# Kernel optimization log

Measured on AMD Instinct MI355X. Metric: run time of the kernel, lower is better.

## Reference

```python
import jax, jax.numpy as jnp
import numpy as np

LAMBDA = 10.0
BETA = 10.0
W = 5  # window size per axis (5,5,5); padding=2 hardcoded in original
DN = ('NCDHW', 'OIDHW', 'NCDHW')


def box_mean(x):
    """Uniform 5x5x5 box-filter mean with zero padding=2, via separable 1D convs."""
    specs = [((1, 1, W, 1, 1), [(2, 2), (0, 0), (0, 0)]),
             ((1, 1, 1, W, 1), [(0, 0), (2, 2), (0, 0)]),
             ((1, 1, 1, 1, W), [(0, 0), (0, 0), (2, 2)])]
    for kshape, pads in specs:
        k = jnp.full(kshape, 1.0 / W, dtype=x.dtype)
        x = jax.lax.conv_general_dilated(x, k, (1, 1, 1), pads, dimension_numbers=DN)
    return x


def lcc_loss(gt, pred):
    omega = gt.size
    d_gt = gt - box_mean(gt)
    d_pred = pred - box_mean(pred)
    num = jnp.square(jnp.sum(d_gt * d_pred))
    den = jnp.sum(jnp.square(d_gt)) * jnp.sum(jnp.square(d_pred))
    den = jnp.maximum(den, 1e-5)
    return -(1.0 / omega) * (num / den)


def reg_field_loss(reg_gt, reg_pred):
    omega = reg_gt.size
    return jnp.sqrt(jnp.sum(jnp.square(reg_pred - reg_gt))) / omega


def tversky_loss2(seg_gt, seg_pred):
    den = jnp.maximum(jnp.sum(seg_gt + seg_pred), 1e-5)
    return -0.5 * jnp.sum(2.0 * seg_gt * seg_pred) / den


def setup_inputs() -> dict:
    key = jax.random.key(0)
    ks = jax.random.split(key, 10)
    shp_f = (2, 3, 128, 128, 128)
    shp_i = (2, 1, 128, 128, 128)
    return {
        'F_0': jax.random.normal(ks[0], shp_f, jnp.float32),
        'F_0g': jax.random.normal(ks[1], shp_f, jnp.float32),
        'I_0': jax.random.uniform(ks[2], shp_i, jnp.float32),
        'I_0R': jax.random.uniform(ks[3], shp_i, jnp.float32),
        'I_1': jax.random.uniform(ks[4], shp_i, jnp.float32),
        'I_1R': jax.random.uniform(ks[5], shp_i, jnp.float32),
        'S_0': jax.random.uniform(ks[6], shp_i, jnp.float32),
        'S_0g': jax.random.uniform(ks[7], shp_i, jnp.float32),
        'S_1': jax.random.uniform(ks[8], shp_i, jnp.float32),
        'S_1g': jax.random.uniform(ks[9], shp_i, jnp.float32),
    }


def reference(F_0, F_0g, I_0, I_0R, I_1, I_1R, S_0, S_0g, S_1, S_1g):
    return (reg_field_loss(F_0, F_0g)
            + LAMBDA * (lcc_loss(I_0, I_0R) + lcc_loss(I_1, I_1R))
            + BETA * (tversky_loss2(S_0, S_0g) + tversky_loss2(S_1, S_1g)))
```

## Files before the change

kernel.cpp:

```cpp
#include <hip/hip_runtime.h>
#include <math.h>

#define VOL   (128*128*128)
#define PLANE (128*128)

#define LCC_BLOCKS   1024
#define SQ_BLOCKS    1024
#define TV_BLOCKS    256
#define TOTAL_BLOCKS (LCC_BLOCKS + SQ_BLOCKS + 2 * TV_BLOCKS)

__device__ __forceinline__ void bar_lds_only() {
    asm volatile("s_waitcnt lgkmcnt(0)");
    __builtin_amdgcn_s_barrier();
}


__device__ __forceinline__ double wave_reduce_d(double v) {
    #pragma unroll
    for (int off = 32; off > 0; off >>= 1)
        v += __shfl_down(v, off, 64);
    return v;
}

__device__ __forceinline__ void block_reduce1_atomic(double a, double* dst) {
    __shared__ double s1[4];
    int lane = threadIdx.x & 63;
    int wave = threadIdx.x >> 6;
    a = wave_reduce_d(a);
    if (lane == 0) s1[wave] = a;
    __syncthreads();
    if (threadIdx.x == 0) {
        double A = s1[0] + s1[1] + s1[2] + s1[3];
        atomicAdd(&dst[0], A);
    }
}

__device__ __forceinline__ void block_reduce2_atomic(double a, double b, double* dst) {
    __shared__ double s2[2][4];
    int lane = threadIdx.x & 63;
    int wave = threadIdx.x >> 6;
    a = wave_reduce_d(a);
    b = wave_reduce_d(b);
    if (lane == 0) { s2[0][wave] = a; s2[1][wave] = b; }
    __syncthreads();
    if (threadIdx.x == 0) {
        atomicAdd(&dst[0], s2[0][0] + s2[0][1] + s2[0][2] + s2[0][3]);
        atomicAdd(&dst[1], s2[1][0] + s2[1][1] + s2[1][2] + s2[1][3]);
    }
}

__device__ __forceinline__ void block_reduce3_atomic(double a, double b, double c, double* dst) {
    __shared__ double s3[3][4];
    int lane = threadIdx.x & 63;
    int wave = threadIdx.x >> 6;
    a = wave_reduce_d(a);
    b = wave_reduce_d(b);
    c = wave_reduce_d(c);
    if (lane == 0) { s3[0][wave] = a; s3[1][wave] = b; s3[2][wave] = c; }
    __syncthreads();
    if (threadIdx.x == 0) {
        atomicAdd(&dst[0], s3[0][0] + s3[0][1] + s3[0][2] + s3[0][3]);
        atomicAdd(&dst[1], s3[1][0] + s3[1][1] + s3[1][2] + s3[1][3]);
        atomicAdd(&dst[2], s3[2][0] + s3[2][1] + s3[2][2] + s3[2][3]);
    }
}


__global__ void zero_ws_kernel(double* ws) {
    if (threadIdx.x < 16) ws[threadIdx.x] = 0.0;
}


__global__ __launch_bounds__(256) void mega_kernel(
    const float* __restrict__ F0,  const float* __restrict__ F0g,
    const float* __restrict__ I0,  const float* __restrict__ I0R,
    const float* __restrict__ I1,  const float* __restrict__ I1R,
    const float* __restrict__ S0,  const float* __restrict__ S0g,
    const float* __restrict__ S1,  const float* __restrict__ S1g,
    double* __restrict__ ws)
{
    int b = blockIdx.x;
    int tid = threadIdx.x;

    if (b < LCC_BLOCKS) {
        __shared__ float ybuf[2 * 8 * 128];
        __shared__ float dbuf[8 * 128];

        int pair = b >> 9;
        int r  = b & 511;
        int y0 = (r & 15) << 3;
        int z0 = ((r >> 4) & 15) << 3;
        int n  = r >> 8;

        const float* gt = pair ? I1  : I0;
        const float* pr = pair ? I1R : I0R;
        double* dst = ws + (pair ? 4 : 1);

        int x = tid & 127;
        int g = tid >> 7;
        const float* V = (g ? pr : gt) + (size_t)n * VOL;

        float a1 = 0.f, a2 = 0.f, a3 = 0.f;
        float ps[5][8];
        float cent1[8], cent2[8];
        float v[12];

        float* yb = ybuf + g * 1024;

        {
            int zp = z0 - 2;
            bool zin = (zp >= 0);
            #pragma unroll
            for (int j = 0; j < 12; ++j) {
                int gy = y0 - 2 + j;
                v[j] = (zin && gy >= 0 && gy < 128)
                         ? V[(size_t)zp * PLANE + (size_t)gy * 128 + x] : 0.0f;
            }
        }

        #pragma unroll
        for (int it = 0; it < 12; ++it) {
            int zp = z0 - 2 + it;

            float vn[12];
            if (it < 11) {
                int zq = zp + 1;
                bool zok = (zq >= 0) && (zq < 128);
                #pragma unroll
                for (int j = 0; j < 12; ++j) {
                    int gy = y0 - 2 + j;
                    vn[j] = (zok && gy >= 0 && gy < 128)
                              ? V[(size_t)zq * PLANE + (size_t)gy * 128 + x] : 0.0f;
                }
            }

            #pragma unroll
            for (int k = 0; k < 8; ++k)
                yb[k * 128 + x] = v[k] + v[k+1] + v[k+2] + v[k+3] + v[k+4];

            bar_lds_only();

            #pragma unroll
            for (int k = 0; k < 8; ++k) {
                float s = yb[k * 128 + x];
                if (x >= 2)   s += yb[k * 128 + x - 2];
                if (x >= 1)   s += yb[k * 128 + x - 1];
                if (x <= 126) s += yb[k * 128 + x + 1];
                if (x <= 125) s += yb[k * 128 + x + 2];
                ps[it % 5][k] = s;
            }

            float d[8];
            if (it >= 4) {
                #pragma unroll
                for (int k = 0; k < 8; ++k) {
                    float m = (ps[0][k] + ps[1][k] + ps[2][k] + ps[3][k] + ps[4][k])
                              * (1.0f / 125.0f);
                    d[k] = cent2[k] - m;
                }
                if (g) {
                    #pragma unroll
                    for (int k = 0; k < 8; ++k) {
                        dbuf[k * 128 + x] = d[k];
                        a3 += d[k] * d[k];
                    }
                }
            }

            bar_lds_only();

            if (it >= 4 && g == 0) {
                #pragma unroll
                for (int k = 0; k < 8; ++k) {
                    float dp = dbuf[k * 128 + x];
                    a1 += d[k] * dp;
                    a2 += d[k] * d[k];
                }
            }

            #pragma unroll
            for (int k = 0; k < 8; ++k) { cent2[k] = cent1[k]; cent1[k] = v[k + 2]; }
            if (it < 11) {
                #pragma unroll
                for (int j = 0; j < 12; ++j) v[j] = vn[j];
            }
        }
        block_reduce3_atomic((double)a1, (double)a2, (double)a3, dst);

    } else if (b < LCC_BLOCKS + SQ_BLOCKS) {
        int bid = b - LCC_BLOCKS;
        const float4* A = (const float4*)F0;
        const float4* B = (const float4*)F0g;
        int n4 = 12582912 / 4;
        int idx = bid * 256 + tid;
        int stride = SQ_BLOCKS * 256;
        float acc = 0.f;
        #pragma unroll 4
        for (int i = idx; i < n4; i += stride) {
            float4 xx = A[i], yy = B[i];
            float d0 = yy.x - xx.x, d1 = yy.y - xx.y;
            float d2 = yy.z - xx.z, d3 = yy.w - xx.w;
            acc += (d0 * d0 + d1 * d1) + (d2 * d2 + d3 * d3);
        }
        block_reduce1_atomic((double)acc, &ws[0]);

    } else {
        int bid = b - (LCC_BLOCKS + SQ_BLOCKS);
        int pair = bid >= TV_BLOCKS;
        bid -= pair ? TV_BLOCKS : 0;
        const float4* Gp = (const float4*)(pair ? S1 : S0);
        const float4* Pp = (const float4*)(pair ? S1g : S0g);
        double* dst = ws + (pair ? 9 : 7);
        int n4 = 4194304 / 4;
        int idx = bid * 256 + tid;
        int stride = TV_BLOCKS * 256;
        float asum = 0.f, aprod = 0.f;
        #pragma unroll 4
        for (int i = idx; i < n4; i += stride) {
            float4 xx = Gp[i], yy = Pp[i];
            asum  += (xx.x + yy.x) + (xx.y + yy.y) + (xx.z + yy.z) + (xx.w + yy.w);
            aprod += (xx.x * yy.x + xx.y * yy.y) + (xx.z * yy.z + xx.w * yy.w);
        }
        block_reduce2_atomic((double)asum, (double)aprod, dst);
    }
}

__global__ void finalize_kernel(const double* __restrict__ ws, float* out) {
    if (threadIdx.x == 0 && blockIdx.x == 0) {
        double reg = sqrt(ws[0]) / 12582912.0;

        double num0 = ws[1] * ws[1];
        double den0 = ws[2] * ws[3];
        if (den0 < 1e-5) den0 = 1e-5;
        double l0 = -(1.0 / 4194304.0) * (num0 / den0);

        double num1 = ws[4] * ws[4];
        double den1 = ws[5] * ws[6];
        if (den1 < 1e-5) den1 = 1e-5;
        double l1 = -(1.0 / 4194304.0) * (num1 / den1);

        double td0 = ws[7]; if (td0 < 1e-5) td0 = 1e-5;
        double t0 = -ws[8] / td0;
        double td1 = ws[9]; if (td1 < 1e-5) td1 = 1e-5;
        double t1 = -ws[10] / td1;

        out[0] = (float)(reg + 10.0 * (l0 + l1) + 10.0 * (t0 + t1));
    }
}


extern "C" void kernel_launch(void* const* d_in, const int* in_sizes, int n_in,
                              void* d_out, int out_size, void* d_ws, size_t ws_size,
                              hipStream_t stream) {
    double* ws = (double*)d_ws;
    float* out = (float*)d_out;

    const float* F0  = (const float*)d_in[0];
    const float* F0g = (const float*)d_in[1];
    const float* I0  = (const float*)d_in[2];
    const float* I0R = (const float*)d_in[3];
    const float* I1  = (const float*)d_in[4];
    const float* I1R = (const float*)d_in[5];
    const float* S0  = (const float*)d_in[6];
    const float* S0g = (const float*)d_in[7];
    const float* S1  = (const float*)d_in[8];
    const float* S1g = (const float*)d_in[9];

    zero_ws_kernel<<<1, 64, 0, stream>>>(ws);
    mega_kernel<<<TOTAL_BLOCKS, 256, 0, stream>>>(F0, F0g, I0, I0R, I1, I1R,
                                                  S0, S0g, S1, S1g, ws);
    finalize_kernel<<<1, 64, 0, stream>>>(ws, out);
}
```

Before: 270.7 us.

## Interleave gt/pred lanes and use shuffles instead of LDS exchange barrier

Gt and pred threads for the same x column are now interleaved as adjacent lanes, so the product of deviations is exchanged with a lane shuffle instead of an LDS buffer and a second barrier per z step. The y-sum buffer is double-buffered across iterations so a single barrier per step suffices, and each thread keeps its own center y-sum in registers to save one LDS read. The global loads now have pairs of lanes reading the same address, which halves effective coalescing width. Accumulation uses mask multiplies to avoid divergence.

```diff
diff --git a/kernel.cpp b/kernel.cpp
--- a/kernel.cpp
+++ b/kernel.cpp
@@ -10,7 +10,7 @@
 #define TOTAL_BLOCKS (LCC_BLOCKS + SQ_BLOCKS + 2 * TV_BLOCKS)
 
 __device__ __forceinline__ void bar_lds_only() {
-    asm volatile("s_waitcnt lgkmcnt(0)");
+    asm volatile("s_waitcnt lgkmcnt(0)" ::: "memory");
     __builtin_amdgcn_s_barrier();
 }
 
@@ -83,8 +83,7 @@
     int tid = threadIdx.x;
 
     if (b < LCC_BLOCKS) {
-        __shared__ float ybuf[2 * 8 * 128];
-        __shared__ float dbuf[8 * 128];
+        __shared__ float ybuf[2][2][8][128];
 
         int pair = b >> 9;
         int r  = b & 511;
@@ -96,16 +95,16 @@
         const float* pr = pair ? I1R : I0R;
         double* dst = ws + (pair ? 4 : 1);
 
-        int x = tid & 127;
-        int g = tid >> 7;
+        int g  = tid & 1;
+        int xp = tid >> 1;
         const float* V = (g ? pr : gt) + (size_t)n * VOL;
+        const float gm  = g ? 0.0f : 1.0f;
+        const float gmi = g ? 1.0f : 0.0f;
 
         float a1 = 0.f, a2 = 0.f, a3 = 0.f;
         float ps[5][8];
         float cent1[8], cent2[8];
-        float v[12];
-
-        float* yb = ybuf + g * 1024;
+        float v[12], ybk[8];
 
         {
             int zp = z0 - 2;
@@ -114,7 +113,7 @@
             for (int j = 0; j < 12; ++j) {
                 int gy = y0 - 2 + j;
                 v[j] = (zin && gy >= 0 && gy < 128)
-                         ? V[(size_t)zp * PLANE + (size_t)gy * 128 + x] : 0.0f;
+                         ? V[(size_t)zp * PLANE + (size_t)gy * 128 + xp] : 0.0f;
             }
         }
 
@@ -130,51 +129,42 @@
                 for (int j = 0; j < 12; ++j) {
                     int gy = y0 - 2 + j;
                     vn[j] = (zok && gy >= 0 && gy < 128)
-                              ? V[(size_t)zq * PLANE + (size_t)gy * 128 + x] : 0.0f;
+                              ? V[(size_t)zq * PLANE + (size_t)gy * 128 + xp] : 0.0f;
                 }
             }
 
-            #pragma unroll
-            for (int k = 0; k < 8; ++k)
-                yb[k * 128 + x] = v[k] + v[k+1] + v[k+2] + v[k+3] + v[k+4];
+            float* yb = &ybuf[it & 1][g][0][0];
+            #pragma unroll
+            for (int k = 0; k < 8; ++k) {
+                float s = v[k] + v[k+1] + v[k+2] + v[k+3] + v[k+4];
+                ybk[k] = s;
+                yb[k * 128 + xp] = s;
+            }
 
             bar_lds_only();
 
             #pragma unroll
             for (int k = 0; k < 8; ++k) {
-                float s = yb[k * 128 + x];
-                if (x >= 2)   s += yb[k * 128 + x - 2];
-                if (x >= 1)   s += yb[k * 128 + x - 1];
-                if (x <= 126) s += yb[k * 128 + x + 1];
-                if (x <= 125) s += yb[k * 128 + x + 2];
+                float s = ybk[k];
+                if (xp >= 2)   s += yb[k * 128 + xp - 2];
+                if (xp >= 1)   s += yb[k * 128 + xp - 1];
+                if (xp <= 126) s += yb[k * 128 + xp + 1];
+                if (xp <= 125) s += yb[k * 128 + xp + 2];
                 ps[it % 5][k] = s;
             }
 
-            float d[8];
             if (it >= 4) {
                 #pragma unroll
                 for (int k = 0; k < 8; ++k) {
                     float m = (ps[0][k] + ps[1][k] + ps[2][k] + ps[3][k] + ps[4][k])
                               * (1.0f / 125.0f);
-                    d[k] = cent2[k] - m;
-                }
-                if (g) {
-                    #pragma unroll
-                    for (int k = 0; k < 8; ++k) {
-                        dbuf[k * 128 + x] = d[k];
-                        a3 += d[k] * d[k];
-                    }
-                }
-            }
-
-            bar_lds_only();
-
-            if (it >= 4 && g == 0) {
-                #pragma unroll
-                for (int k = 0; k < 8; ++k) {
-                    float dp = dbuf[k * 128 + x];
-                    a1 += d[k] * dp;
-                    a2 += d[k] * d[k];
+                    float d  = cent2[k] - m;
+                    float dp = __shfl_xor(d, 1, 64);
+                    float prod = d * dp;
+                    float sq   = d * d;
+                    a1 += prod * gm;
+                    a2 += sq   * gm;
+                    a3 += sq   * gmi;
                 }
             }
 
```

Result: slower. 282.7 us (+4.4%).

## Deepen z-plane prefetch to two planes and remap LCC block order

Applied to the files above, without the earlier changes.

The LCC stencil loop now keeps a three-slot register ring of z-planes and prefetches two planes ahead instead of one, so global loads have more iterations to land before use. It also keeps the center y-sum in registers instead of re-reading it from LDS, adds a memory clobber to the LDS barrier asm, and permutes the block index so consecutive blocks cover different tiles. The deeper prefetch raises register pressure and may lower occupancy, and the block permutation changes the cache and XCD locality pattern.

```diff
diff --git a/kernel.cpp b/kernel.cpp
--- a/kernel.cpp
+++ b/kernel.cpp
@@ -10,7 +10,7 @@
 #define TOTAL_BLOCKS (LCC_BLOCKS + SQ_BLOCKS + 2 * TV_BLOCKS)
 
 __device__ __forceinline__ void bar_lds_only() {
-    asm volatile("s_waitcnt lgkmcnt(0)");
+    asm volatile("s_waitcnt lgkmcnt(0)" ::: "memory");
     __builtin_amdgcn_s_barrier();
 }
 
@@ -86,8 +86,10 @@
         __shared__ float ybuf[2 * 8 * 128];
         __shared__ float dbuf[8 * 128];
 
-        int pair = b >> 9;
-        int r  = b & 511;
+        int L = (b & 7) * 128 + (b >> 3);
+
+        int pair = L >> 9;
+        int r  = L & 511;
         int y0 = (r & 15) << 3;
         int z0 = ((r >> 4) & 15) << 3;
         int n  = r >> 8;
@@ -103,46 +105,52 @@
         float a1 = 0.f, a2 = 0.f, a3 = 0.f;
         float ps[5][8];
         float cent1[8], cent2[8];
-        float v[12];
+        float vp[3][12];
+        float ybk[8];
 
         float* yb = ybuf + g * 1024;
 
-        {
-            int zp = z0 - 2;
+        #pragma unroll
+        for (int s = 0; s < 2; ++s) {
+            int zp = z0 - 2 + s;
             bool zin = (zp >= 0);
             #pragma unroll
             for (int j = 0; j < 12; ++j) {
                 int gy = y0 - 2 + j;
-                v[j] = (zin && gy >= 0 && gy < 128)
-                         ? V[(size_t)zp * PLANE + (size_t)gy * 128 + x] : 0.0f;
+                vp[s][j] = (zin && gy >= 0 && gy < 128)
+                             ? V[(size_t)zp * PLANE + (size_t)gy * 128 + x] : 0.0f;
             }
         }
 
         #pragma unroll
         for (int it = 0; it < 12; ++it) {
-            int zp = z0 - 2 + it;
-
-            float vn[12];
-            if (it < 11) {
-                int zq = zp + 1;
-                bool zok = (zq >= 0) && (zq < 128);
+            const int cur = it % 3;
+            const int nxt = (it + 2) % 3;
+
+            if (it < 10) {
+                int zq = z0 + it;
+                bool zok = (zq < 128);
                 #pragma unroll
                 for (int j = 0; j < 12; ++j) {
                     int gy = y0 - 2 + j;
-                    vn[j] = (zok && gy >= 0 && gy < 128)
-                              ? V[(size_t)zq * PLANE + (size_t)gy * 128 + x] : 0.0f;
-                }
-            }
-
-            #pragma unroll
-            for (int k = 0; k < 8; ++k)
-                yb[k * 128 + x] = v[k] + v[k+1] + v[k+2] + v[k+3] + v[k+4];
+                    vp[nxt][j] = (zok && gy >= 0 && gy < 128)
+                                   ? V[(size_t)zq * PLANE + (size_t)gy * 128 + x] : 0.0f;
+                }
+            }
+
+            #pragma unroll
+            for (int k = 0; k < 8; ++k) {
+                float s = vp[cur][k] + vp[cur][k+1] + vp[cur][k+2]
+                        + vp[cur][k+3] + vp[cur][k+4];
+                ybk[k] = s;
+                yb[k * 128 + x] = s;
+            }
 
             bar_lds_only();
 
             #pragma unroll
             for (int k = 0; k < 8; ++k) {
-                float s = yb[k * 128 + x];
+                float s = ybk[k];
                 if (x >= 2)   s += yb[k * 128 + x - 2];
                 if (x >= 1)   s += yb[k * 128 + x - 1];
                 if (x <= 126) s += yb[k * 128 + x + 1];
@@ -179,11 +187,7 @@
             }
 
             #pragma unroll
-            for (int k = 0; k < 8; ++k) { cent2[k] = cent1[k]; cent1[k] = v[k + 2]; }
-            if (it < 11) {
-                #pragma unroll
-                for (int j = 0; j < 12; ++j) v[j] = vn[j];
-            }
+            for (int k = 0; k < 8; ++k) { cent2[k] = cent1[k]; cent1[k] = vp[cur][k + 2]; }
         }
         block_reduce3_atomic((double)a1, (double)a2, (double)a3, dst);
 
```

Measured after the change: 260.8 us. 1.04x faster.
